# Kernel tuning notes

Hardware: AMD Instinct MI355X
Metric: run time of the kernel (lower is better)

Reference implementation:

```python
import jax, jax.numpy as jnp
import numpy as np
import math

N = 10000      # atoms
E = 320000     # neighbor pairs (edges)
NELEM = 3      # species one-hot size
NRAD = 8       # radial channels per component
NB = 8         # bessel basis size
ZETA = 4       # max angular moment
RC = 5.0       # radial cutoff
S = 4          # species embedding size (species_layer_sizes[-1])
NCOMP = (ZETA + 2) * NRAD   # 2-body slice + (ZETA+1) angular slices = 48
FEAT = NCOMP * S            # 192

# multinomial expansion of (r_i . r_j)^l : lxlylz powers and l!/(lx!ly!lz!) norms
_TERMS = []
for l in range(ZETA + 1):
    pw, nm = [], []
    for a in range(l + 1):
        for b in range(l + 1 - a):
            c = l - a - b
            pw.append((a, b, c))
            nm.append(math.factorial(l) / (math.factorial(a) * math.factorial(b) * math.factorial(c)))
    _TERMS.append((np.array(pw, dtype=np.float32), np.array(nm, dtype=np.float32)))


def _silu(x):
    return x * jax.nn.sigmoid(x)


def setup_inputs() -> dict:
    key = jax.random.key(0)
    ks = jax.random.split(key, 12)
    rij = (jax.random.uniform(ks[0], (E, 3), minval=-1.0, maxval=1.0) * (RC / math.sqrt(3.0))).astype(jnp.float32)
    first_atom = jax.random.randint(ks[1], (E,), 0, N, dtype=jnp.int32)
    second_atom = jax.random.randint(ks[2], (E,), 0, N, dtype=jnp.int32)
    species_idx = jax.random.randint(ks[3], (N,), 0, NELEM, dtype=jnp.int32)
    w = lambda k, s: (jax.random.normal(k, s) * 0.1).astype(jnp.float32)
    z = lambda s: jnp.zeros(s, jnp.float32)
    return dict(
        rij=rij, species_idx=species_idx, first_atom=first_atom, second_atom=second_atom,
        Wr1=w(ks[4], (NB, 64)), br1=z((64,)),
        Wr2=w(ks[5], (64, NCOMP)), br2=z((NCOMP,)),
        Ws1=w(ks[6], (NELEM, 16)), bs1=z((16,)),
        Ws2=w(ks[7], (16, S)), bs2=z((S,)),
        Wa1=w(ks[8], (FEAT, 64)), ba1=z((64,)),
        Wa2=w(ks[9], (64, 64)), ba2=z((64,)),
        Wa3=w(ks[10], (64, 1)), ba3=z((1,)),
    )


def reference(rij, species_idx, first_atom, second_atom,
              Wr1, br1, Wr2, br2, Ws1, bs1, Ws2, bs2,
              Wa1, ba1, Wa2, ba2, Wa3, ba3):
    d = jnp.sqrt(jnp.sum(rij * rij, axis=-1) + 1e-12)            # [E]
    rhat = rij / d[:, None]                                       # [E,3]
    fc = jnp.where(d < RC, 0.5 * (jnp.cos(np.pi * d / RC) + 1.0), 0.0)
    n = jnp.arange(1, NB + 1, dtype=rij.dtype)
    bes = jnp.sqrt(2.0 / RC) * jnp.sin(n[None, :] * np.pi * d[:, None] / RC) / d[:, None]  # [E,NB]
    # learned radial functions, all components at once, smoothed by cutoff
    R = _silu(_silu(bes @ Wr1 + br1) @ Wr2 + br2) * fc[:, None]   # [E, NCOMP]
    # species encoder -> per-atom embedding, gathered on neighbor atom j
    onehot = jax.nn.one_hot(species_idx, NELEM, dtype=rij.dtype)  # [N,NELEM]
    semb = jnp.tanh(onehot @ Ws1 + bs1) @ Ws2 + bs2               # [N,S]
    sj = semb[second_atom]                                        # [E,S]
    # 2-body feature
    feats = [jax.ops.segment_sum(R[:, :NRAD, None] * sj[:, None, :], first_atom, num_segments=N)]  # [N,NRAD,S]
    off = NRAD
    for l in range(ZETA + 1):
        pw, nm = _TERMS[l]
        comps = jnp.prod(rhat[:, None, :] ** jnp.asarray(pw)[None, :, :], axis=-1)  # [E,C_l]
        Rl = R[:, off:off + NRAD]
        off += NRAD
        edge = Rl[:, :, None, None] * comps[:, None, :, None] * sj[:, None, None, :]  # [E,NRAD,C_l,S]
        A = jax.ops.segment_sum(edge, first_atom, num_segments=N)                     # [N,NRAD,C_l,S]
        feats.append(jnp.einsum('nrcs,c->nrs', A * A, jnp.asarray(nm)))               # [N,NRAD,S]
    feat = jnp.concatenate(feats, axis=1).reshape(N, -1)          # [N, FEAT]
    h = _silu(feat @ Wa1 + ba1)
    h = _silu(h @ Wa2 + ba2)
    return (h @ Wa3 + ba3)[:, 0]                                  # per-atom energies [N]
```

## Files before the change

### kernel.cpp

```cpp
#include <hip/hip_runtime.h>
#include <math.h>

#define NATOMS 10000
#define NEDGES 320000
#define NBINS  (NATOMS * 4)
#define RC_F 5.0f
#define PI_F 3.14159265358979323846f

#define WS_SEMB   0
#define WS_GTOT   12
#define WS_CNT    16
#define WS_OFFS   40016
#define WS_CURSOR 80016
#define WS_EIDX   120016
#define WS_SA     440096
#define WS_SB     10680096

__device__ __constant__ int   d_PWA[35] = {0, 0,0,1, 0,0,0,1,1,2, 0,0,0,0,1,1,1,2,2,3, 0,0,0,0,0,1,1,1,1,2,2,2,3,3,4};
__device__ __constant__ int   d_PWB[35] = {0, 0,1,0, 0,1,2,0,1,0, 0,1,2,3,0,1,2,0,1,0, 0,1,2,3,4,0,1,2,3,0,1,2,0,1,0};
__device__ __constant__ int   d_PWC[35] = {0, 1,0,0, 2,1,0,1,0,0, 3,2,1,0,2,1,0,1,0,0, 4,3,2,1,0,3,2,1,0,2,1,0,1,0,0};
__device__ __constant__ float d_NM[35]  = {1.f, 1.f,1.f,1.f, 1.f,2.f,1.f,2.f,2.f,1.f,
                                           1.f,3.f,3.f,1.f,3.f,6.f,3.f,3.f,3.f,1.f,
                                           1.f,4.f,6.f,4.f,1.f,4.f,12.f,12.f,4.f,6.f,12.f,6.f,4.f,4.f,1.f};
__device__ __constant__ int   d_LBLK[35]= {0, 1,1,1, 2,2,2,2,2,2, 3,3,3,3,3,3,3,3,3,3, 4,4,4,4,4,4,4,4,4,4,4,4,4,4,4};
__device__ __constant__ int   d_L6[6]   = {0,1,4,10,20,35};

__device__ __forceinline__ float siluf(float x) { return x / (1.0f + __expf(-x)); }

__device__ __forceinline__ float2 f2fma(float2 a, float2 b, float2 c) {
  return make_float2(fmaf(a.x, b.x, c.x), fmaf(a.y, b.y, c.y));
}

__device__ __forceinline__ float psel(float x, int p) {
  float x2 = x * x;
  float r = 1.0f;
  r = (p == 1) ? x : r;
  r = (p == 2) ? x2 : r;
  r = (p == 3) ? x2 * x : r;
  r = (p == 4) ? x2 * x2 : r;
  return r;
}

__global__ void k_init(const float* __restrict__ Ws1, const float* __restrict__ bs1,
                       const float* __restrict__ Ws2, const float* __restrict__ bs2,
                       float* __restrict__ ws)
{
  int tid = blockIdx.x * blockDim.x + threadIdx.x;
  int* cnt = (int*)(ws + WS_CNT);
  if (tid < NBINS) cnt[tid] = 0;
  if (tid == 0) *(int*)(ws + WS_GTOT) = 0;
  if (tid < 12) {
    int t = tid >> 2, s = tid & 3;
    float acc = bs2[s];
    for (int j = 0; j < 16; j++) acc += tanhf(Ws1[t * 16 + j] + bs1[j]) * Ws2[j * 4 + s];
    ws[WS_SEMB + tid] = acc;
  }
}

__global__ void k_hist(const int* __restrict__ first_atom, const int* __restrict__ second_atom,
                       const int* __restrict__ species, float* __restrict__ ws)
{
  int e = blockIdx.x * blockDim.x + threadIdx.x;
  if (e < NEDGES) {
    int* cnt = (int*)(ws + WS_CNT);
    int bin = first_atom[e] * 4 + species[second_atom[e]];
    atomicAdd(&cnt[bin], 1);
  }
}

__global__ __launch_bounds__(256) void k_alloc(float* __restrict__ ws)
{
  const int4* cnt4 = (const int4*)(ws + WS_CNT);
  int4* offs4   = (int4*)(ws + WS_OFFS);
  int4* cursor4 = (int4*)(ws + WS_CURSOR);
  int* gtot = (int*)(ws + WS_GTOT);
  __shared__ int wsum[4];
  __shared__ int sbase;
  int tid = threadIdx.x;
  int lane = tid & 63, wv = tid >> 6;
  int a = blockIdx.x * 256 + tid;
  bool live = (a < NATOMS);
  int4 c = live ? cnt4[a] : make_int4(0, 0, 0, 0);
  int s = c.x + c.y + c.z + c.w;
  int inc = s;
  #pragma unroll
  for (int d = 1; d < 64; d <<= 1) {
    int v = __shfl_up(inc, d, 64);
    if (lane >= d) inc += v;
  }
  if (lane == 63) wsum[wv] = inc;
  __syncthreads();
  if (tid == 0) sbase = atomicAdd(gtot, wsum[0] + wsum[1] + wsum[2] + wsum[3]);
  __syncthreads();
  int woff = sbase;
  for (int w = 0; w < wv; w++) woff += wsum[w];
  int o0 = woff + inc - s;
  if (live) {
    int4 o;
    o.x = o0;
    o.y = o.x + c.x;
    o.z = o.y + c.y;
    o.w = o.z + c.z;
    offs4[a] = o;
    cursor4[a] = o;
  }
}

__global__ __launch_bounds__(256) void k_edge(
    const float* __restrict__ rij, const int* __restrict__ species,
    const int* __restrict__ first_atom, const int* __restrict__ second_atom,
    const float* __restrict__ Wr1, const float* __restrict__ br1,
    const float* __restrict__ Wr2, const float* __restrict__ br2,
    float* __restrict__ ws)
{
  __shared__ __align__(16) float sRec[4][64 * 28];
  int tid = threadIdx.x, lane = tid & 63, wv = tid >> 6;
  int e = blockIdx.x * 256 + tid;
  int* cursor = (int*)(ws + WS_CURSOR);
  int* eidx   = (int*)(ws + WS_EIDX);
  float* myrow = &sRec[wv][lane * 28];

  int a = first_atom[e];
  int t = species[second_atom[e]];
  int pos = atomicAdd(&cursor[a * 4 + t], 1);
  eidx[pos] = e;

  float x = rij[e * 3 + 0], y = rij[e * 3 + 1], z = rij[e * 3 + 2];
  float d = sqrtf(x * x + y * y + z * z + 1e-12f);
  float invd = 1.0f / d;

  float theta = (PI_F / RC_F) * d;
  float s1 = __sinf(theta), c1 = __cosf(theta);
  float fc = (d < RC_F) ? 0.5f * (c1 + 1.0f) : 0.0f;
  float bes[8];
  {
    float sq = sqrtf(2.0f / RC_F) * invd;
    float twoc = 2.0f * c1;
    float sp = 0.0f, sc = s1;
    #pragma unroll
    for (int k = 0; k < 8; k++) {
      bes[k] = sq * sc;
      float sn = twoc * sc - sp;
      sp = sc; sc = sn;
    }
  }

  float h1[64];
  #pragma unroll
  for (int j4 = 0; j4 < 16; j4++) {
    float2 a01 = *(const float2*)&br1[j4 * 4];
    float2 a23 = *(const float2*)&br1[j4 * 4 + 2];
    #pragma unroll
    for (int k = 0; k < 8; k++) {
      float2 b2 = make_float2(bes[k], bes[k]);
      a01 = f2fma(b2, *(const float2*)&Wr1[k * 64 + j4 * 4],     a01);
      a23 = f2fma(b2, *(const float2*)&Wr1[k * 64 + j4 * 4 + 2], a23);
    }
    h1[j4 * 4 + 0] = siluf(a01.x);
    h1[j4 * 4 + 1] = siluf(a01.y);
    h1[j4 * 4 + 2] = siluf(a23.x);
    h1[j4 * 4 + 3] = siluf(a23.y);
  }

  int ebase = blockIdx.x * 256 + wv * 64;
  const float* buf = &sRec[wv][0];
  int f4 = lane & 7;

  for (int j4 = 0; j4 < 6; j4++) {
    float2 a01 = *(const float2*)&br2[j4 * 4];
    float2 a23 = *(const float2*)&br2[j4 * 4 + 2];
    #pragma unroll
    for (int k = 0; k < 64; k++) {
      float2 h2 = make_float2(h1[k], h1[k]);
      a01 = f2fma(h2, *(const float2*)&Wr2[k * 48 + j4 * 4],     a01);
      a23 = f2fma(h2, *(const float2*)&Wr2[k * 48 + j4 * 4 + 2], a23);
    }
    *(float4*)(myrow + j4 * 4) = make_float4(siluf(a01.x) * fc, siluf(a01.y) * fc,
                                             siluf(a23.x) * fc, siluf(a23.y) * fc);
  }
  {
    float* gbase = ws + WS_SA + (size_t)ebase * 32;
    if (f4 < 6) {
      #pragma unroll
      for (int q = 0; q < 8; q++) {
        int g4 = q * 64 + lane;
        float4 v = *(const float4*)(buf + (g4 >> 3) * 28 + f4 * 4);
        *(float4*)(gbase + (size_t)g4 * 4) = v;
      }
    }
  }

  for (int j4 = 6; j4 < 12; j4++) {
    float2 a01 = *(const float2*)&br2[j4 * 4];
    float2 a23 = *(const float2*)&br2[j4 * 4 + 2];
    #pragma unroll
    for (int k = 0; k < 64; k++) {
      float2 h2 = make_float2(h1[k], h1[k]);
      a01 = f2fma(h2, *(const float2*)&Wr2[k * 48 + j4 * 4],     a01);
      a23 = f2fma(h2, *(const float2*)&Wr2[k * 48 + j4 * 4 + 2], a23);
    }
    *(float4*)(myrow + (j4 - 6) * 4) = make_float4(siluf(a01.x) * fc, siluf(a01.y) * fc,
                                                   siluf(a23.x) * fc, siluf(a23.y) * fc);
  }
  *(float4*)(myrow + 24) = make_float4(x * invd, y * invd, z * invd, 0.0f);
  {
    float* gbase = ws + WS_SB + (size_t)ebase * 32;
    if (f4 < 7) {
      #pragma unroll
      for (int q = 0; q < 8; q++) {
        int g4 = q * 64 + lane;
        float4 v = *(const float4*)(buf + (g4 >> 3) * 28 + f4 * 4);
        *(float4*)(gbase + (size_t)g4 * 4) = v;
      }
    }
  }
}

__global__ __launch_bounds__(128) void k_atom(
    const float* __restrict__ ws,
    const float* __restrict__ Wa1, const float* __restrict__ ba1,
    const float* __restrict__ Wa2, const float* __restrict__ ba2,
    const float* __restrict__ Wa3, const float* __restrict__ ba3,
    float* __restrict__ out)
{
  __shared__ __align__(16) float sScr[2][1920];
  int tid = threadIdx.x;
  int lane = tid & 63, wv = tid >> 6;
  int a = blockIdx.x * 2 + wv;
  float* sStage = &sScr[wv][0];
  float* sG     = &sScr[wv][768];
  float* sFeat  = &sScr[wv][1632];
  float* sH     = &sScr[wv][1824];

  const int* eidx = (const int*)(ws + WS_EIDX);
  int4 o = ((const int4*)(ws + WS_OFFS))[a];

  const int c = lane;
  bool isc = (c < 35);
  int pa = 0, pb = 0, pcw = 0, lb = 0;
  if (isc) { pa = d_PWA[c]; pb = d_PWB[c]; pcw = d_PWC[c]; lb = d_LBLK[c]; }
  int rdir = lane - 35;
  bool isd = (rdir >= 0) && (rdir < 8);
  int rl = lane >> 4, fl = lane & 15;
  const float* gsrc = ws + (fl < 6 ? WS_SA : WS_SB);
  int foff = (fl < 6) ? fl : ((fl < 13) ? fl - 6 : 6);

  float2 g2[3][4];
  #pragma unroll
  for (int t2 = 0; t2 < 3; t2++)
    #pragma unroll
    for (int r = 0; r < 4; r++) g2[t2][r] = make_float2(0.f, 0.f);
  float g0[3] = {0.0f, 0.0f, 0.0f};

#define CORE(T) {                                                             \
    const float* rb = buf + j * 64;                                           \
    if (isc) {                                                                \
      float comp = psel(rb[48], pa) * psel(rb[49], pb) * psel(rb[50], pcw);   \
      float2 c2 = make_float2(comp, comp);                                    \
      const float2* r2 = (const float2*)(rb + 8 + 8 * lb);                    \
      g2[T][0] = f2fma(c2, r2[0], g2[T][0]);                                  \
      g2[T][1] = f2fma(c2, r2[1], g2[T][1]);                                  \
      g2[T][2] = f2fma(c2, r2[2], g2[T][2]);                                  \
      g2[T][3] = f2fma(c2, r2[3], g2[T][3]);                                  \
    } else if (isd) {                                                         \
      g0[T] += rb[rdir];                                                      \
    }                                                                         \
  }

#define LOADR(Q, DST) {                                                       \
    int sl_ = (Q) * 4 + rl; if (sl_ >= m) sl_ = m - 1;                        \
    int pk_ = __shfl(packed, sl_, 64);                                        \
    DST = *(const float4*)(gsrc + (size_t)pk_ * 32 + foff * 4);               \
  }

#define RUN(T, LO, HI)                                                        \
  for (int cb = (LO); cb < (HI); cb += 64) {                                  \
    int m = (HI) - cb; if (m > 64) m = 64;                                    \
    int pp = cb + lane;                                                       \
    int packed = eidx[pp < (HI) ? pp : (LO)];                                 \
    int R = (m + 3) >> 2;                                                     \
    float4 v0, v1;                                                            \
    LOADR(0, v0)                                                              \
    if (R > 1) { LOADR(1, v1) } else v1 = v0;                                 \
    int bsel = 0;                                                             \
    for (int r = 0; r < R; r++) {                                             \
      float* buf = sStage + (bsel << 8);                                      \
      bsel = (bsel == 2) ? 0 : bsel + 1;                                      \
      *(float4*)(buf + rl * 64 + fl * 4) = v0;                                \
      v0 = v1;                                                                \
      if (r + 2 < R) LOADR(r + 2, v1)                                         \
      int g = r * 4, gm = m - g; if (gm > 4) gm = 4;                          \
      for (int j = 0; j < gm; j++) CORE(T)                                    \
    }                                                                         \
  }

  RUN(0, o.x, o.y)
  RUN(1, o.y, o.z)
  RUN(2, o.z, o.w)
#undef RUN
#undef CORE
#undef LOADR

  if (isc) {
    #pragma unroll
    for (int t2 = 0; t2 < 3; t2++)
      #pragma unroll
      for (int r = 0; r < 8; r++) {
        float gval = (r & 1) ? g2[t2][r >> 1].y : g2[t2][r >> 1].x;
        sG[(t2 * 8 + r) * 36 + c] = gval;
      }
  } else if (isd) {
    #pragma unroll
    for (int t2 = 0; t2 < 3; t2++) sG[(t2 * 8 + rdir) * 36 + 35] = g0[t2];
  }

  int s = lane & 3;
  float se0 = ws[WS_SEMB + s], se1 = ws[WS_SEMB + 4 + s], se2 = ws[WS_SEMB + 8 + s];
  float fout[3];
  #pragma unroll
  for (int u = 0; u < 3; u++) {
    int f = lane + 64 * u;
    int blk = f >> 5, rr = (f >> 2) & 7;
    float acc;
    if (blk == 0) {
      acc = se0 * sG[(0 + rr) * 36 + 35] + se1 * sG[(8 + rr) * 36 + 35] + se2 * sG[(16 + rr) * 36 + 35];
    } else {
      int c0 = d_L6[blk - 1], c1 = d_L6[blk];
      acc = 0.0f;
      for (int cc = c0; cc < c1; cc++) {
        float A = se0 * sG[(0 + rr) * 36 + cc] + se1 * sG[(8 + rr) * 36 + cc] + se2 * sG[(16 + rr) * 36 + cc];
        acc += d_NM[cc] * A * A;
      }
    }
    fout[u] = acc;
  }
  #pragma unroll
  for (int u = 0; u < 3; u++) sFeat[lane + 64 * u] = fout[u];

  {
    float a0 = 0.f, a1 = 0.f, a2 = 0.f, a3 = 0.f;
    for (int k4 = 0; k4 < 48; k4++) {
      float4 f4 = *(const float4*)(sFeat + k4 * 4);
      const float* w = Wa1 + (k4 * 4) * 64 + lane;
      a0 += f4.x * w[0];
      a1 += f4.y * w[64];
      a2 += f4.z * w[128];
      a3 += f4.w * w[192];
    }
    sH[lane] = siluf(a0 + a1 + a2 + a3 + ba1[lane]);
  }

  {
    float a0 = 0.f, a1 = 0.f, a2 = 0.f, a3 = 0.f;
    for (int k4 = 0; k4 < 16; k4++) {
      float4 h4 = *(const float4*)(sH + k4 * 4);
      const float* w = Wa2 + (k4 * 4) * 64 + lane;
      a0 += h4.x * w[0];
      a1 += h4.y * w[64];
      a2 += h4.z * w[128];
      a3 += h4.w * w[192];
    }
    float h2 = siluf(a0 + a1 + a2 + a3 + ba2[lane]);
    float pr = h2 * Wa3[lane];
    #pragma unroll
    for (int off = 32; off > 0; off >>= 1) pr += __shfl_down(pr, off, 64);
    if (lane == 0) out[a] = pr + ba3[0];
  }
}

extern "C" void kernel_launch(void* const* d_in, const int* in_sizes, int n_in,
                              void* d_out, int out_size, void* d_ws, size_t ws_size,
                              hipStream_t stream)
{
  const float* rij         = (const float*)d_in[0];
  const int*   species     = (const int*)  d_in[1];
  const int*   first_atom  = (const int*)  d_in[2];
  const int*   second_atom = (const int*)  d_in[3];
  const float* Wr1 = (const float*)d_in[4];
  const float* br1 = (const float*)d_in[5];
  const float* Wr2 = (const float*)d_in[6];
  const float* br2 = (const float*)d_in[7];
  const float* Ws1 = (const float*)d_in[8];
  const float* bs1 = (const float*)d_in[9];
  const float* Ws2 = (const float*)d_in[10];
  const float* bs2 = (const float*)d_in[11];
  const float* Wa1 = (const float*)d_in[12];
  const float* ba1 = (const float*)d_in[13];
  const float* Wa2 = (const float*)d_in[14];
  const float* ba2 = (const float*)d_in[15];
  const float* Wa3 = (const float*)d_in[16];
  const float* ba3 = (const float*)d_in[17];
  float* ws  = (float*)d_ws;
  float* out = (float*)d_out;

  k_init<<<(NBINS + 255) / 256, 256, 0, stream>>>(Ws1, bs1, Ws2, bs2, ws);
  k_hist<<<(NEDGES + 255) / 256, 256, 0, stream>>>(first_atom, second_atom, species, ws);
  k_alloc<<<(NATOMS + 255) / 256, 256, 0, stream>>>(ws);
  k_edge<<<NEDGES / 256, 256, 0, stream>>>(rij, species, first_atom, second_atom,
                                           Wr1, br1, Wr2, br2, ws);
  k_atom<<<NATOMS / 2, 128, 0, stream>>>(ws, Wa1, ba1, Wa2, ba2, Wa3, ba3, out);
}
```

Baseline: 211.4 us.

## Write edge records directly at sorted bucket positions, dropping the index indirection

The edge kernel now scatters each edge's radial and direction record straight to its counting-sort slot (pos) in global memory. It no longer stages records through shared memory and writes them in edge order along with an eidx permutation array. The atom kernel then reads records contiguously by slot instead of loading eidx and shuffling indices, which removes one dependent gather level and the eidx traffic. The cost is that the edge kernel's stores become scattered per-thread float4 writes rather than coalesced tile writes.

Result: slower. 221.9 us (+5.0%).

```diff
diff --git a/kernel.cpp b/kernel.cpp
--- a/kernel.cpp
+++ b/kernel.cpp
@@ -113,17 +113,12 @@
     const float* __restrict__ Wr2, const float* __restrict__ br2,
     float* __restrict__ ws)
 {
-  __shared__ __align__(16) float sRec[4][64 * 28];
-  int tid = threadIdx.x, lane = tid & 63, wv = tid >> 6;
-  int e = blockIdx.x * 256 + tid;
+  int e = blockIdx.x * 256 + threadIdx.x;
   int* cursor = (int*)(ws + WS_CURSOR);
-  int* eidx   = (int*)(ws + WS_EIDX);
-  float* myrow = &sRec[wv][lane * 28];
 
   int a = first_atom[e];
   int t = species[second_atom[e]];
   int pos = atomicAdd(&cursor[a * 4 + t], 1);
-  eidx[pos] = e;
 
   float x = rij[e * 3 + 0], y = rij[e * 3 + 1], z = rij[e * 3 + 2];
   float d = sqrtf(x * x + y * y + z * z + 1e-12f);
@@ -162,9 +157,8 @@
     h1[j4 * 4 + 3] = siluf(a23.y);
   }
 
-  int ebase = blockIdx.x * 256 + wv * 64;
-  const float* buf = &sRec[wv][0];
-  int f4 = lane & 7;
+  float* recA = ws + WS_SA + (size_t)pos * 32;
+  float* recB = ws + WS_SB + (size_t)pos * 32;
 
   for (int j4 = 0; j4 < 6; j4++) {
     float2 a01 = *(const float2*)&br2[j4 * 4];
@@ -175,19 +169,8 @@
       a01 = f2fma(h2, *(const float2*)&Wr2[k * 48 + j4 * 4],     a01);
       a23 = f2fma(h2, *(const float2*)&Wr2[k * 48 + j4 * 4 + 2], a23);
     }
-    *(float4*)(myrow + j4 * 4) = make_float4(siluf(a01.x) * fc, siluf(a01.y) * fc,
-                                             siluf(a23.x) * fc, siluf(a23.y) * fc);
-  }
-  {
-    float* gbase = ws + WS_SA + (size_t)ebase * 32;
-    if (f4 < 6) {
-      #pragma unroll
-      for (int q = 0; q < 8; q++) {
-        int g4 = q * 64 + lane;
-        float4 v = *(const float4*)(buf + (g4 >> 3) * 28 + f4 * 4);
-        *(float4*)(gbase + (size_t)g4 * 4) = v;
-      }
-    }
+    *(float4*)(recA + j4 * 4) = make_float4(siluf(a01.x) * fc, siluf(a01.y) * fc,
+                                            siluf(a23.x) * fc, siluf(a23.y) * fc);
   }
 
   for (int j4 = 6; j4 < 12; j4++) {
@@ -199,21 +182,10 @@
       a01 = f2fma(h2, *(const float2*)&Wr2[k * 48 + j4 * 4],     a01);
       a23 = f2fma(h2, *(const float2*)&Wr2[k * 48 + j4 * 4 + 2], a23);
     }
-    *(float4*)(myrow + (j4 - 6) * 4) = make_float4(siluf(a01.x) * fc, siluf(a01.y) * fc,
-                                                   siluf(a23.x) * fc, siluf(a23.y) * fc);
-  }
-  *(float4*)(myrow + 24) = make_float4(x * invd, y * invd, z * invd, 0.0f);
-  {
-    float* gbase = ws + WS_SB + (size_t)ebase * 32;
-    if (f4 < 7) {
-      #pragma unroll
-      for (int q = 0; q < 8; q++) {
-        int g4 = q * 64 + lane;
-        float4 v = *(const float4*)(buf + (g4 >> 3) * 28 + f4 * 4);
-        *(float4*)(gbase + (size_t)g4 * 4) = v;
-      }
-    }
-  }
+    *(float4*)(recB + (j4 - 6) * 4) = make_float4(siluf(a01.x) * fc, siluf(a01.y) * fc,
+                                                  siluf(a23.x) * fc, siluf(a23.y) * fc);
+  }
+  *(float4*)(recB + 24) = make_float4(x * invd, y * invd, z * invd, 0.0f);
 }
 
 __global__ __launch_bounds__(128) void k_atom(
@@ -232,7 +204,6 @@
   float* sFeat  = &sScr[wv][1632];
   float* sH     = &sScr[wv][1824];
 
-  const int* eidx = (const int*)(ws + WS_EIDX);
   int4 o = ((const int4*)(ws + WS_OFFS))[a];
 
   const int c = lane;
@@ -269,15 +240,12 @@
 
 #define LOADR(Q, DST) {                                                       \
     int sl_ = (Q) * 4 + rl; if (sl_ >= m) sl_ = m - 1;                        \
-    int pk_ = __shfl(packed, sl_, 64);                                        \
-    DST = *(const float4*)(gsrc + (size_t)pk_ * 32 + foff * 4);               \
+    DST = *(const float4*)(gsrc + (size_t)(cb + sl_) * 32 + foff * 4);        \
   }
 
 #define RUN(T, LO, HI)                                                        \
   for (int cb = (LO); cb < (HI); cb += 64) {                                  \
     int m = (HI) - cb; if (m > 64) m = 64;                                    \
-    int pp = cb + lane;                                                       \
-    int packed = eidx[pp < (HI) ? pp : (LO)];                                 \
     int R = (m + 3) >> 2;                                                     \
     float4 v0, v1;                                                            \
     LOADR(0, v0)                                                              \
```
